# Optimization experiments

Hardware: AMD Instinct MI355X
Metric: run time of the kernel (lower is better)

## Reference

```python
import jax, jax.numpy as jnp
import numpy as np

HEADS = 16
DIM = 1024
D_K = DIM // HEADS
SEQ = 2048


def setup_inputs() -> dict:
    key = jax.random.key(0)
    ks = jax.random.split(key, 11)
    s = 1.0 / np.sqrt(DIM).astype(np.float32)
    return {
        "q": jax.random.normal(ks[0], (SEQ, DIM), jnp.float32),
        "k": jax.random.normal(ks[1], (SEQ, DIM), jnp.float32),
        "v": jax.random.normal(ks[2], (SEQ, DIM), jnp.float32),
        "Wq": jax.random.normal(ks[3], (DIM, DIM), jnp.float32) * s,
        "bq": jax.random.normal(ks[4], (DIM,), jnp.float32) * 0.01,
        "Wk": jax.random.normal(ks[5], (DIM, DIM), jnp.float32) * s,
        "bk": jax.random.normal(ks[6], (DIM,), jnp.float32) * 0.01,
        "Wv": jax.random.normal(ks[7], (DIM, DIM), jnp.float32) * s,
        "bv": jax.random.normal(ks[8], (DIM,), jnp.float32) * 0.01,
        "Wo": jax.random.normal(ks[9], (DIM, DIM), jnp.float32) * s,
        "bo": jax.random.normal(ks[10], (DIM,), jnp.float32) * 0.01,
    }


def reference(q, k, v, Wq, bq, Wk, bk, Wv, bv, Wo, bo):
    S = q.shape[0]
    # torch Linear: x @ W.T + b; view to (1, S, H, d_k) then transpose to (1, H, S, d_k)
    def proj(x, W, b):
        return (x @ W.T + b).reshape(1, S, HEADS, D_K).transpose(0, 2, 1, 3)

    qh = proj(q, Wq, bq)  # (1, H, S, d)
    kh = proj(k, Wk, bk)
    vh = proj(v, Wv, bv)

    scale = 1.0 / np.sqrt(D_K).astype(np.float32)
    scores = jnp.einsum("bhqd,bhkd->bhqk", qh, kh) * scale  # (1, H, S, S)
    # NOTE: source applies softmax over dim=1 == the HEADS axis (faithful quirk)
    attn = jax.nn.softmax(scores, axis=1)
    ctx = jnp.einsum("bhqk,bhkd->bhqd", attn, vh)  # (1, H, S, d)
    concat = ctx.transpose(0, 2, 1, 3).reshape(1, S, DIM)
    return concat @ Wo.T + bo
```

## Files before the change

kernel.cpp:

```cpp
#include <hip/hip_runtime.h>
#include <hip/hip_fp16.h>


typedef _Float16 f16;
typedef _Float16 f16x4 __attribute__((ext_vector_type(4)));
typedef _Float16 f16x8 __attribute__((ext_vector_type(8)));
typedef float    f32x4 __attribute__((ext_vector_type(4)));

#define S_LEN 2048
#define DIM   1024
#define NH    16
#define DK    64
#define SCALE 0.125f

#define MFMA(a, b, c) __builtin_amdgcn_mfma_f32_16x16x32_f16(a, b, c, 0, 0, 0)

typedef __attribute__((address_space(1))) void g_void;
typedef __attribute__((address_space(3))) void l_void;

static __device__ __forceinline__ void gload_lds16(const void* g, void* l) {
  __builtin_amdgcn_global_load_lds((g_void*)g, (l_void*)l, 16, 0, 0);
}

__global__ __launch_bounds__(256) void cvt_f32_f16(const float* __restrict__ src,
                                                   f16* __restrict__ dst, int n4) {
  int i = blockIdx.x * 256 + threadIdx.x;
  if (i < n4) {
    float4 v = ((const float4*)src)[i];
    f16x4 o = {(f16)v.x, (f16)v.y, (f16)v.z, (f16)v.w};
    ((f16x4*)dst)[i] = o;
  }
}

__global__ __launch_bounds__(256) void cvt3(const float* __restrict__ s0, const float* __restrict__ s1,
                                            const float* __restrict__ s2, f16* __restrict__ d0,
                                            f16* __restrict__ d1, f16* __restrict__ d2, int n4) {
  int z = blockIdx.y;
  const float* src = z == 0 ? s0 : z == 1 ? s1 : s2;
  f16* dst = z == 0 ? d0 : z == 1 ? d1 : d2;
  int i = blockIdx.x * 256 + threadIdx.x;
  if (i < n4) {
    float4 v = ((const float4*)src)[i];
    f16x4 o = {(f16)v.x, (f16)v.y, (f16)v.z, (f16)v.w};
    ((f16x4*)dst)[i] = o;
  }
}

__global__ __launch_bounds__(256) void cvt4(const float* __restrict__ s0, const float* __restrict__ s1,
                                            const float* __restrict__ s2, const float* __restrict__ s3,
                                            f16* __restrict__ d0, f16* __restrict__ d1,
                                            f16* __restrict__ d2, f16* __restrict__ d3, int n4) {
  int z = blockIdx.y;
  const float* src = z == 0 ? s0 : z == 1 ? s1 : z == 2 ? s2 : s3;
  f16* dst = z == 0 ? d0 : z == 1 ? d1 : z == 2 ? d2 : d3;
  int i = blockIdx.x * 256 + threadIdx.x;
  if (i < n4) {
    float4 v = ((const float4*)src)[i];
    f16x4 o = {(f16)v.x, (f16)v.y, (f16)v.z, (f16)v.w};
    ((f16x4*)dst)[i] = o;
  }
}

static __device__ __forceinline__ void gemm64_core(const f16* __restrict__ X,
                                                   const f16* __restrict__ W,
                                                   int k0, int k1, int bm, int bn,
                                                   f16* As, f16* Bs,
                                                   f32x4 (&acc)[4][2]) {
  const int tid = threadIdx.x;
  const int wv = tid >> 6;
  const int lane = tid & 63;
  const int qd = lane >> 4;
  const int l16 = lane & 15;
  const int wm = (wv & 1) * 64;
  const int wn = (wv >> 1) * 32;
  const int lr4 = lane >> 2, lc4 = lane & 3;

  const f16* gA = X + (size_t)(bm + wv * 32 + lr4) * DIM + k0 + lc4 * 8;
  const f16* gB = W + (size_t)(bn + wv * 16 + lr4) * DIM + k0 + lc4 * 8;
  f16* lA = &As[(wv * 32) * 32];
  f16* lB = &Bs[(wv * 16) * 32];

  for (int kt = k0; kt < k1; kt += 32) {
    gload_lds16(gA, lA);
    gload_lds16(gA + 16 * DIM, lA + 16 * 32);
    gload_lds16(gB, lB);
    gA += 32;
    gB += 32;
    __syncthreads();

    f16x8 af[4], bf[2];
#pragma unroll
    for (int mi = 0; mi < 4; mi++)
      af[mi] = *(const f16x8*)&As[(wm + mi * 16 + l16) * 32 + qd * 8];
#pragma unroll
    for (int ni = 0; ni < 2; ni++)
      bf[ni] = *(const f16x8*)&Bs[(wn + ni * 16 + l16) * 32 + qd * 8];
#pragma unroll
    for (int mi = 0; mi < 4; mi++)
#pragma unroll
      for (int ni = 0; ni < 2; ni++)
        acc[mi][ni] = MFMA(af[mi], bf[ni], acc[mi][ni]);
    __syncthreads();
  }
}

__global__ __launch_bounds__(256) void gemm_qkv(
    const f16* __restrict__ X0, const f16* __restrict__ X1, const f16* __restrict__ X2,
    const f16* __restrict__ W0, const f16* __restrict__ W1, const f16* __restrict__ W2,
    const float* __restrict__ b0, const float* __restrict__ b1, const float* __restrict__ b2,
    f16* __restrict__ o0, f16* __restrict__ o1, f16* __restrict__ o2) {
  __shared__ __align__(16) f16 As[128 * 32];
  __shared__ __align__(16) f16 Bs[64 * 32];
  const int z = blockIdx.z;
  const f16* X = z == 0 ? X0 : z == 1 ? X1 : X2;
  const f16* W = z == 0 ? W0 : z == 1 ? W1 : W2;
  const float* bias = z == 0 ? b0 : z == 1 ? b1 : b2;
  f16* outh = z == 0 ? o0 : z == 1 ? o1 : o2;

  const int bm = blockIdx.y * 128, bn = blockIdx.x * 64;
  f32x4 acc[4][2];
#pragma unroll
  for (int a = 0; a < 4; a++)
#pragma unroll
    for (int b = 0; b < 2; b++) acc[a][b] = (f32x4){0.f, 0.f, 0.f, 0.f};

  gemm64_core(X, W, 0, DIM, bm, bn, As, Bs, acc);

  const int tid = threadIdx.x;
  const int wv = tid >> 6, lane = tid & 63;
  const int qd = lane >> 4, l16 = lane & 15;
  const int wm = (wv & 1) * 64, wn = (wv >> 1) * 32;
#pragma unroll
  for (int mi = 0; mi < 4; mi++) {
#pragma unroll
    for (int ni = 0; ni < 2; ni++) {
      const int gm = bm + wm + mi * 16 + qd * 4;
      const int gn = bn + wn + ni * 16 + l16;
      const float bs = bias[gn];
      if (z == 2) {
        f16x4 o = {(f16)(acc[mi][ni][0] + bs), (f16)(acc[mi][ni][1] + bs),
                   (f16)(acc[mi][ni][2] + bs), (f16)(acc[mi][ni][3] + bs)};
        *(f16x4*)&outh[(size_t)gn * S_LEN + gm] = o;
      } else {
#pragma unroll
        for (int r = 0; r < 4; r++)
          outh[(size_t)(gm + r) * DIM + gn] = (f16)(acc[mi][ni][r] + bs);
      }
    }
  }
}

__global__ __launch_bounds__(256) void gemm_out(const f16* __restrict__ X,
                                                const f16* __restrict__ W,
                                                const float* __restrict__ bias,
                                                float* __restrict__ outf) {
  __shared__ __align__(16) f16 As[128 * 32];
  __shared__ __align__(16) f16 Bs[64 * 32];
  const int z = blockIdx.z;
  const int bm = blockIdx.y * 128, bn = blockIdx.x * 64;
  f32x4 acc[4][2];
#pragma unroll
  for (int a = 0; a < 4; a++)
#pragma unroll
    for (int b = 0; b < 2; b++) acc[a][b] = (f32x4){0.f, 0.f, 0.f, 0.f};

  gemm64_core(X, W, z * (DIM / 2), (z + 1) * (DIM / 2), bm, bn, As, Bs, acc);

  const int tid = threadIdx.x;
  const int wv = tid >> 6, lane = tid & 63;
  const int qd = lane >> 4, l16 = lane & 15;
  const int wm = (wv & 1) * 64, wn = (wv >> 1) * 32;
#pragma unroll
  for (int mi = 0; mi < 4; mi++) {
#pragma unroll
    for (int ni = 0; ni < 2; ni++) {
      const int gm = bm + wm + mi * 16 + qd * 4;
      const int gn = bn + wn + ni * 16 + l16;
      const float bs = z == 0 ? bias[gn] : 0.f;
#pragma unroll
      for (int r = 0; r < 4; r++)
        atomicAdd(&outf[(size_t)(gm + r) * DIM + gn], acc[mi][ni][r] + bs);
    }
  }
}

__global__ __launch_bounds__(256) void attn_denom(const f16* __restrict__ Qp,
                                                  const f16* __restrict__ Kp,
                                                  f16* __restrict__ IDn) {
  __shared__ __align__(16) f16 Qs[2][64 * 32];
  __shared__ __align__(16) f16 Ks[2][64 * 32];
  const int tid = threadIdx.x;
  const int wv = tid >> 6;
  const int lane = tid & 63;
  const int qd = lane >> 4;
  const int l16 = lane & 15;
  const int wm = (wv & 1) * 32, wn = (wv >> 1) * 32;
  const int bi = blockIdx.y * 64, bj = blockIdx.x * 64;
  const int lr4 = lane >> 2, lc4 = lane & 3;
  const int kkw = wv & 1;
  const int rw = (wv >> 1) * 32;

  f32x4 dsum[2][2];
#pragma unroll
  for (int a = 0; a < 2; a++)
#pragma unroll
    for (int b = 0; b < 2; b++) dsum[a][b] = (f32x4){0.f, 0.f, 0.f, 0.f};

  for (int h = 0; h < NH; h++) {
    const f16* gq = Qp + (size_t)(bi + rw + lr4) * DIM + h * DK + kkw * 32 + lc4 * 8;
    const f16* gk = Kp + (size_t)(bj + rw + lr4) * DIM + h * DK + kkw * 32 + lc4 * 8;
    gload_lds16(gq, &Qs[kkw][rw * 32]);
    gload_lds16(gq + 16 * DIM, &Qs[kkw][(rw + 16) * 32]);
    gload_lds16(gk, &Ks[kkw][rw * 32]);
    gload_lds16(gk + 16 * DIM, &Ks[kkw][(rw + 16) * 32]);
    __syncthreads();

    f16x8 af[2][2], bf[2][2];
#pragma unroll
    for (int mi = 0; mi < 2; mi++)
#pragma unroll
      for (int kk = 0; kk < 2; kk++)
        af[mi][kk] = *(const f16x8*)&Qs[kk][(wm + mi * 16 + l16) * 32 + qd * 8];
#pragma unroll
    for (int ni = 0; ni < 2; ni++)
#pragma unroll
      for (int kk = 0; kk < 2; kk++)
        bf[ni][kk] = *(const f16x8*)&Ks[kk][(wn + ni * 16 + l16) * 32 + qd * 8];
#pragma unroll
    for (int mi = 0; mi < 2; mi++)
#pragma unroll
      for (int ni = 0; ni < 2; ni++) {
        f32x4 s = {0.f, 0.f, 0.f, 0.f};
        s = MFMA(af[mi][0], bf[ni][0], s);
        s = MFMA(af[mi][1], bf[ni][1], s);
#pragma unroll
        for (int r = 0; r < 4; r++) dsum[mi][ni][r] += __expf(s[r] * SCALE);
      }
    __syncthreads();
  }
#pragma unroll
  for (int mi = 0; mi < 2; mi++)
#pragma unroll
    for (int ni = 0; ni < 2; ni++)
#pragma unroll
      for (int r = 0; r < 4; r++) {
        const int gi = bi + wm + mi * 16 + qd * 4 + r;
        const int gj = bj + wn + ni * 16 + l16;
        IDn[(size_t)gi * S_LEN + gj] = (f16)(1.f / dsum[mi][ni][r]);
      }
}

__global__ __launch_bounds__(256) void attn_ctx(const f16* __restrict__ Qp,
                                                const f16* __restrict__ Kp,
                                                const f16* __restrict__ Vt,
                                                const f16* __restrict__ IDn,
                                                float* __restrict__ Cp) {
  __shared__ __align__(16) f16 Ks[2][32 * 32];
  __shared__ __align__(16) f16 Vs[64 * 32];
  __shared__ __align__(16) f16 Is[128 * 32];
  __shared__ __align__(16) f16 Pl[4][32 * 32];
  const int tid = threadIdx.x;
  const int wv = tid >> 6;
  const int lane = tid & 63;
  const int qd = lane >> 4;
  const int l16 = lane & 15;
  const int h = blockIdx.y;
  const int i0 = blockIdx.x * 128;
  const int iw = i0 + wv * 32;
  const int jb = blockIdx.z * 512;
  const int lr4 = lane >> 2, lc4 = lane & 3;
  f16* pl = Pl[wv];

  f16x8 aq[2][2];
#pragma unroll
  for (int mi = 0; mi < 2; mi++)
#pragma unroll
    for (int kk = 0; kk < 2; kk++)
      aq[mi][kk] = *(const f16x8*)(Qp + (size_t)(iw + mi * 16 + l16) * DIM +
                                   h * DK + kk * 32 + qd * 8);

  f32x4 acc[2][4];
#pragma unroll
  for (int a = 0; a < 2; a++)
#pragma unroll
    for (int b = 0; b < 4; b++) acc[a][b] = (f32x4){0.f, 0.f, 0.f, 0.f};

  for (int jt = 0; jt < 16; jt++) {
    const int j0 = jb + jt * 32;
    gload_lds16(Kp + (size_t)(j0 + (wv >> 1) * 16 + lr4) * DIM + h * DK + (wv & 1) * 32 + lc4 * 8,
                &Ks[wv & 1][((wv >> 1) * 16) * 32]);
    gload_lds16(Vt + (size_t)(h * DK + wv * 16 + lr4) * S_LEN + j0 + lc4 * 8,
                &Vs[(wv * 16) * 32]);
#pragma unroll
    for (int t = 0; t < 2; t++) {
      const int row = (wv * 2 + t) * 16;
      gload_lds16(IDn + (size_t)(i0 + row + lr4) * S_LEN + j0 + lc4 * 8,
                  &Is[row * 32]);
    }
    __syncthreads();

    f16x8 bk[2][2];
#pragma unroll
    for (int ni = 0; ni < 2; ni++)
#pragma unroll
      for (int kk = 0; kk < 2; kk++)
        bk[ni][kk] = *(const f16x8*)&Ks[kk][(ni * 16 + l16) * 32 + qd * 8];
#pragma unroll
    for (int mi = 0; mi < 2; mi++)
#pragma unroll
      for (int ni = 0; ni < 2; ni++) {
        f32x4 s = {0.f, 0.f, 0.f, 0.f};
        s = MFMA(aq[mi][0], bk[ni][0], s);
        s = MFMA(aq[mi][1], bk[ni][1], s);
#pragma unroll
        for (int r = 0; r < 4; r++)
          pl[(mi * 16 + qd * 4 + r) * 32 + ni * 16 + l16] = (f16)__expf(s[r] * SCALE);
      }

    f16x8 bv[4];
#pragma unroll
    for (int nd = 0; nd < 4; nd++)
      bv[nd] = *(const f16x8*)&Vs[(nd * 16 + l16) * 32 + qd * 8];
#pragma unroll
    for (int mi = 0; mi < 2; mi++) {
      f16x8 ef = *(const f16x8*)&pl[(mi * 16 + l16) * 32 + qd * 8];
      f16x8 idn = *(const f16x8*)&Is[(wv * 32 + mi * 16 + l16) * 32 + qd * 8];
      f16x8 p = ef * idn;
#pragma unroll
      for (int nd = 0; nd < 4; nd++)
        acc[mi][nd] = MFMA(p, bv[nd], acc[mi][nd]);
    }
    __syncthreads();
  }

#pragma unroll
  for (int mi = 0; mi < 2; mi++)
#pragma unroll
    for (int nd = 0; nd < 4; nd++)
#pragma unroll
      for (int r = 0; r < 4; r++)
        atomicAdd(&Cp[(size_t)(iw + mi * 16 + qd * 4 + r) * DIM + h * DK + nd * 16 + l16],
                  acc[mi][nd][r]);
}

extern "C" void kernel_launch(void* const* d_in, const int* in_sizes, int n_in,
                              void* d_out, int out_size, void* d_ws, size_t ws_size,
                              hipStream_t stream) {
  const float* q  = (const float*)d_in[0];
  const float* k  = (const float*)d_in[1];
  const float* v  = (const float*)d_in[2];
  const float* Wq = (const float*)d_in[3];
  const float* bq = (const float*)d_in[4];
  const float* Wk = (const float*)d_in[5];
  const float* bk = (const float*)d_in[6];
  const float* Wv = (const float*)d_in[7];
  const float* bv = (const float*)d_in[8];
  const float* Wo = (const float*)d_in[9];
  const float* bo = (const float*)d_in[10];
  float* out = (float*)d_out;

  f16* w = (f16*)d_ws;
  f16* qh  = w;
  f16* kh  = qh + (size_t)S_LEN * DIM;
  f16* vh  = kh + (size_t)S_LEN * DIM;
  f16* wqh = vh + (size_t)S_LEN * DIM;
  f16* wkh = wqh + (size_t)DIM * DIM;
  f16* wvh = wkh + (size_t)DIM * DIM;
  f16* woh = wvh + (size_t)DIM * DIM;
  f16* Qp  = woh + (size_t)DIM * DIM;
  f16* Kp  = Qp + (size_t)S_LEN * DIM;
  f16* Vt  = Kp + (size_t)S_LEN * DIM;
  f16* IDn = qh;
  float* Cp = (float*)vh;
  f16* Ct  = qh;

  const int nqkv4 = S_LEN * DIM / 4, nw4 = DIM * DIM / 4;
  dim3 b256(256);
  cvt3<<<dim3(nqkv4 / 256, 3), b256, 0, stream>>>(q, k, v, qh, kh, vh, nqkv4);
  cvt4<<<dim3(nw4 / 256, 4), b256, 0, stream>>>(Wq, Wk, Wv, Wo, wqh, wkh, wvh, woh, nw4);

  gemm_qkv<<<dim3(DIM / 64, S_LEN / 128, 3), b256, 0, stream>>>(
      qh, kh, vh, wqh, wkh, wvh, bq, bk, bv, Qp, Kp, Vt);

  hipMemsetAsync(Cp, 0, (size_t)S_LEN * DIM * sizeof(float), stream);
  hipMemsetAsync(out, 0, (size_t)S_LEN * DIM * sizeof(float), stream);

  attn_denom<<<dim3(S_LEN / 64, S_LEN / 64), b256, 0, stream>>>(Qp, Kp, IDn);
  attn_ctx<<<dim3(S_LEN / 128, NH, 4), b256, 0, stream>>>(Qp, Kp, Vt, IDn, Cp);

  cvt_f32_f16<<<nqkv4 / 256, b256, 0, stream>>>(Cp, Ct, nqkv4);

  gemm_out<<<dim3(DIM / 64, S_LEN / 128, 2), b256, 0, stream>>>(Ct, woh, bo, out);
}
```

Before: 235.4 us.

## Double K-step per barrier in GEMM and attention kernels, merge conversion launches

The GEMM core, the attention-denominator kernel and the attention-context kernel now load twice as much data per synchronisation step: 64-wide K in the GEMM, two heads per iteration in attn_denom, and 64 keys per tile in attn_ctx. This halves the number of __syncthreads barriers and loop iterations, at the cost of more LDS per block. The two input conversion kernels are merged into one 10-segment launch to save a kernel launch. The larger LDS footprint may reduce occupancy.

```diff
diff --git a/kernel.cpp b/kernel.cpp
--- a/kernel.cpp
+++ b/kernel.cpp
@@ -20,6 +20,34 @@
 
 static __device__ __forceinline__ void gload_lds16(const void* g, void* l) {
   __builtin_amdgcn_global_load_lds((g_void*)g, (l_void*)l, 16, 0, 0);
+}
+
+__global__ __launch_bounds__(256) void cvt_all(
+    const float* __restrict__ q, const float* __restrict__ k, const float* __restrict__ v,
+    const float* __restrict__ Wq, const float* __restrict__ Wk, const float* __restrict__ Wv,
+    const float* __restrict__ Wo, f16* __restrict__ qh, f16* __restrict__ kh,
+    f16* __restrict__ vh, f16* __restrict__ wqh, f16* __restrict__ wkh,
+    f16* __restrict__ wvh, f16* __restrict__ woh) {
+  const size_t M = 1048576;
+  const int seg = blockIdx.y;
+  const float* src;
+  f16* dst;
+  switch (seg) {
+    case 0: src = q;      dst = qh;      break;
+    case 1: src = q + M;  dst = qh + M;  break;
+    case 2: src = k;      dst = kh;      break;
+    case 3: src = k + M;  dst = kh + M;  break;
+    case 4: src = v;      dst = vh;      break;
+    case 5: src = v + M;  dst = vh + M;  break;
+    case 6: src = Wq;     dst = wqh;     break;
+    case 7: src = Wk;     dst = wkh;     break;
+    case 8: src = Wv;     dst = wvh;     break;
+    default: src = Wo;    dst = woh;     break;
+  }
+  int i = blockIdx.x * 256 + threadIdx.x;
+  float4 vv = ((const float4*)src)[i];
+  f16x4 o = {(f16)vv.x, (f16)vv.y, (f16)vv.z, (f16)vv.w};
+  ((f16x4*)dst)[i] = o;
 }
 
 __global__ __launch_bounds__(256) void cvt_f32_f16(const float* __restrict__ src,
@@ -32,39 +60,10 @@
   }
 }
 
-__global__ __launch_bounds__(256) void cvt3(const float* __restrict__ s0, const float* __restrict__ s1,
-                                            const float* __restrict__ s2, f16* __restrict__ d0,
-                                            f16* __restrict__ d1, f16* __restrict__ d2, int n4) {
-  int z = blockIdx.y;
-  const float* src = z == 0 ? s0 : z == 1 ? s1 : s2;
-  f16* dst = z == 0 ? d0 : z == 1 ? d1 : d2;
-  int i = blockIdx.x * 256 + threadIdx.x;
-  if (i < n4) {
-    float4 v = ((const float4*)src)[i];
-    f16x4 o = {(f16)v.x, (f16)v.y, (f16)v.z, (f16)v.w};
-    ((f16x4*)dst)[i] = o;
-  }
-}
-
-__global__ __launch_bounds__(256) void cvt4(const float* __restrict__ s0, const float* __restrict__ s1,
-                                            const float* __restrict__ s2, const float* __restrict__ s3,
-                                            f16* __restrict__ d0, f16* __restrict__ d1,
-                                            f16* __restrict__ d2, f16* __restrict__ d3, int n4) {
-  int z = blockIdx.y;
-  const float* src = z == 0 ? s0 : z == 1 ? s1 : z == 2 ? s2 : s3;
-  f16* dst = z == 0 ? d0 : z == 1 ? d1 : z == 2 ? d2 : d3;
-  int i = blockIdx.x * 256 + threadIdx.x;
-  if (i < n4) {
-    float4 v = ((const float4*)src)[i];
-    f16x4 o = {(f16)v.x, (f16)v.y, (f16)v.z, (f16)v.w};
-    ((f16x4*)dst)[i] = o;
-  }
-}
-
 static __device__ __forceinline__ void gemm64_core(const f16* __restrict__ X,
                                                    const f16* __restrict__ W,
                                                    int k0, int k1, int bm, int bn,
-                                                   f16* As, f16* Bs,
+                                                   f16* As2, f16* Bs2,
                                                    f32x4 (&acc)[4][2]) {
   const int tid = threadIdx.x;
   const int wv = tid >> 6;
@@ -74,32 +73,43 @@
   const int wm = (wv & 1) * 64;
   const int wn = (wv >> 1) * 32;
   const int lr4 = lane >> 2, lc4 = lane & 3;
-
-  const f16* gA = X + (size_t)(bm + wv * 32 + lr4) * DIM + k0 + lc4 * 8;
-  const f16* gB = W + (size_t)(bn + wv * 16 + lr4) * DIM + k0 + lc4 * 8;
-  f16* lA = &As[(wv * 32) * 32];
-  f16* lB = &Bs[(wv * 16) * 32];
-
-  for (int kt = k0; kt < k1; kt += 32) {
-    gload_lds16(gA, lA);
-    gload_lds16(gA + 16 * DIM, lA + 16 * 32);
-    gload_lds16(gB, lB);
-    gA += 32;
-    gB += 32;
-    __syncthreads();
-
-    f16x8 af[4], bf[2];
+  const int kkw = wv & 1;
+  const int rgw = wv >> 1;
+
+  const f16* gA = X + (size_t)(bm + rgw * 64 + lr4) * DIM + k0 + kkw * 32 + lc4 * 8;
+  const f16* gB = W + (size_t)(bn + rgw * 32 + lr4) * DIM + k0 + kkw * 32 + lc4 * 8;
+  f16* lA = As2 + kkw * (128 * 32) + (rgw * 64) * 32;
+  f16* lB = Bs2 + kkw * (64 * 32) + (rgw * 32) * 32;
+
+  for (int kt = k0; kt < k1; kt += 64) {
+#pragma unroll
+    for (int t = 0; t < 4; t++)
+      gload_lds16(gA + t * 16 * DIM, lA + t * 16 * 32);
+#pragma unroll
+    for (int t = 0; t < 2; t++)
+      gload_lds16(gB + t * 16 * DIM, lB + t * 16 * 32);
+    gA += 64;
+    gB += 64;
+    __syncthreads();
+
+    f16x8 af[4][2], bf[2][2];
 #pragma unroll
     for (int mi = 0; mi < 4; mi++)
-      af[mi] = *(const f16x8*)&As[(wm + mi * 16 + l16) * 32 + qd * 8];
+#pragma unroll
+      for (int kk = 0; kk < 2; kk++)
+        af[mi][kk] = *(const f16x8*)&As2[kk * (128 * 32) + (wm + mi * 16 + l16) * 32 + qd * 8];
 #pragma unroll
     for (int ni = 0; ni < 2; ni++)
-      bf[ni] = *(const f16x8*)&Bs[(wn + ni * 16 + l16) * 32 + qd * 8];
+#pragma unroll
+      for (int kk = 0; kk < 2; kk++)
+        bf[ni][kk] = *(const f16x8*)&Bs2[kk * (64 * 32) + (wn + ni * 16 + l16) * 32 + qd * 8];
 #pragma unroll
     for (int mi = 0; mi < 4; mi++)
 #pragma unroll
-      for (int ni = 0; ni < 2; ni++)
-        acc[mi][ni] = MFMA(af[mi], bf[ni], acc[mi][ni]);
+      for (int ni = 0; ni < 2; ni++) {
+        acc[mi][ni] = MFMA(af[mi][0], bf[ni][0], acc[mi][ni]);
+        acc[mi][ni] = MFMA(af[mi][1], bf[ni][1], acc[mi][ni]);
+      }
     __syncthreads();
   }
 }
@@ -109,8 +119,8 @@
     const f16* __restrict__ W0, const f16* __restrict__ W1, const f16* __restrict__ W2,
     const float* __restrict__ b0, const float* __restrict__ b1, const float* __restrict__ b2,
     f16* __restrict__ o0, f16* __restrict__ o1, f16* __restrict__ o2) {
-  __shared__ __align__(16) f16 As[128 * 32];
-  __shared__ __align__(16) f16 Bs[64 * 32];
+  __shared__ __align__(16) f16 As2[2 * 128 * 32];
+  __shared__ __align__(16) f16 Bs2[2 * 64 * 32];
   const int z = blockIdx.z;
   const f16* X = z == 0 ? X0 : z == 1 ? X1 : X2;
   const f16* W = z == 0 ? W0 : z == 1 ? W1 : W2;
@@ -124,7 +134,7 @@
 #pragma unroll
     for (int b = 0; b < 2; b++) acc[a][b] = (f32x4){0.f, 0.f, 0.f, 0.f};
 
-  gemm64_core(X, W, 0, DIM, bm, bn, As, Bs, acc);
+  gemm64_core(X, W, 0, DIM, bm, bn, As2, Bs2, acc);
 
   const int tid = threadIdx.x;
   const int wv = tid >> 6, lane = tid & 63;
@@ -154,8 +164,8 @@
                                                 const f16* __restrict__ W,
                                                 const float* __restrict__ bias,
                                                 float* __restrict__ outf) {
-  __shared__ __align__(16) f16 As[128 * 32];
-  __shared__ __align__(16) f16 Bs[64 * 32];
+  __shared__ __align__(16) f16 As2[2 * 128 * 32];
+  __shared__ __align__(16) f16 Bs2[2 * 64 * 32];
   const int z = blockIdx.z;
   const int bm = blockIdx.y * 128, bn = blockIdx.x * 64;
   f32x4 acc[4][2];
@@ -164,7 +174,7 @@
 #pragma unroll
     for (int b = 0; b < 2; b++) acc[a][b] = (f32x4){0.f, 0.f, 0.f, 0.f};
 
-  gemm64_core(X, W, z * (DIM / 2), (z + 1) * (DIM / 2), bm, bn, As, Bs, acc);
+  gemm64_core(X, W, z * (DIM / 2), (z + 1) * (DIM / 2), bm, bn, As2, Bs2, acc);
 
   const int tid = threadIdx.x;
   const int wv = tid >> 6, lane = tid & 63;
@@ -187,8 +197,8 @@
 __global__ __launch_bounds__(256) void attn_denom(const f16* __restrict__ Qp,
                                                   const f16* __restrict__ Kp,
                                                   f16* __restrict__ IDn) {
-  __shared__ __align__(16) f16 Qs[2][64 * 32];
-  __shared__ __align__(16) f16 Ks[2][64 * 32];
+  __shared__ __align__(16) f16 Qs[2][2][64 * 32];
+  __shared__ __align__(16) f16 Ks[2][2][64 * 32];
   const int tid = threadIdx.x;
   const int wv = tid >> 6;
   const int lane = tid & 63;
@@ -197,8 +207,8 @@
   const int wm = (wv & 1) * 32, wn = (wv >> 1) * 32;
   const int bi = blockIdx.y * 64, bj = blockIdx.x * 64;
   const int lr4 = lane >> 2, lc4 = lane & 3;
-  const int kkw = wv & 1;
-  const int rw = (wv >> 1) * 32;
+  const int hhw = wv & 1;
+  const int kkw = wv >> 1;
 
   f32x4 dsum[2][2];
 #pragma unroll
@@ -206,36 +216,41 @@
 #pragma unroll
     for (int b = 0; b < 2; b++) dsum[a][b] = (f32x4){0.f, 0.f, 0.f, 0.f};
 
-  for (int h = 0; h < NH; h++) {
-    const f16* gq = Qp + (size_t)(bi + rw + lr4) * DIM + h * DK + kkw * 32 + lc4 * 8;
-    const f16* gk = Kp + (size_t)(bj + rw + lr4) * DIM + h * DK + kkw * 32 + lc4 * 8;
-    gload_lds16(gq, &Qs[kkw][rw * 32]);
-    gload_lds16(gq + 16 * DIM, &Qs[kkw][(rw + 16) * 32]);
-    gload_lds16(gk, &Ks[kkw][rw * 32]);
-    gload_lds16(gk + 16 * DIM, &Ks[kkw][(rw + 16) * 32]);
-    __syncthreads();
-
-    f16x8 af[2][2], bf[2][2];
-#pragma unroll
-    for (int mi = 0; mi < 2; mi++)
-#pragma unroll
-      for (int kk = 0; kk < 2; kk++)
-        af[mi][kk] = *(const f16x8*)&Qs[kk][(wm + mi * 16 + l16) * 32 + qd * 8];
-#pragma unroll
-    for (int ni = 0; ni < 2; ni++)
-#pragma unroll
-      for (int kk = 0; kk < 2; kk++)
-        bf[ni][kk] = *(const f16x8*)&Ks[kk][(wn + ni * 16 + l16) * 32 + qd * 8];
-#pragma unroll
-    for (int mi = 0; mi < 2; mi++)
-#pragma unroll
-      for (int ni = 0; ni < 2; ni++) {
-        f32x4 s = {0.f, 0.f, 0.f, 0.f};
-        s = MFMA(af[mi][0], bf[ni][0], s);
-        s = MFMA(af[mi][1], bf[ni][1], s);
-#pragma unroll
-        for (int r = 0; r < 4; r++) dsum[mi][ni][r] += __expf(s[r] * SCALE);
-      }
+  for (int h0 = 0; h0 < NH; h0 += 2) {
+    const int hcol = (h0 + hhw) * DK + kkw * 32;
+    const f16* gq = Qp + (size_t)(bi + lr4) * DIM + hcol + lc4 * 8;
+    const f16* gk = Kp + (size_t)(bj + lr4) * DIM + hcol + lc4 * 8;
+#pragma unroll
+    for (int t = 0; t < 4; t++) {
+      gload_lds16(gq + (size_t)t * 16 * DIM, &Qs[hhw][kkw][t * 16 * 32]);
+      gload_lds16(gk + (size_t)t * 16 * DIM, &Ks[hhw][kkw][t * 16 * 32]);
+    }
+    __syncthreads();
+
+#pragma unroll
+    for (int hh = 0; hh < 2; hh++) {
+      f16x8 af[2][2], bf[2][2];
+#pragma unroll
+      for (int mi = 0; mi < 2; mi++)
+#pragma unroll
+        for (int kk = 0; kk < 2; kk++)
+          af[mi][kk] = *(const f16x8*)&Qs[hh][kk][(wm + mi * 16 + l16) * 32 + qd * 8];
+#pragma unroll
+      for (int ni = 0; ni < 2; ni++)
+#pragma unroll
+        for (int kk = 0; kk < 2; kk++)
+          bf[ni][kk] = *(const f16x8*)&Ks[hh][kk][(wn + ni * 16 + l16) * 32 + qd * 8];
+#pragma unroll
+      for (int mi = 0; mi < 2; mi++)
+#pragma unroll
+        for (int ni = 0; ni < 2; ni++) {
+          f32x4 s = {0.f, 0.f, 0.f, 0.f};
+          s = MFMA(af[mi][0], bf[ni][0], s);
+          s = MFMA(af[mi][1], bf[ni][1], s);
+#pragma unroll
+          for (int r = 0; r < 4; r++) dsum[mi][ni][r] += __expf(s[r] * SCALE);
+        }
+    }
     __syncthreads();
   }
 #pragma unroll
@@ -255,9 +270,9 @@
                                                 const f16* __restrict__ Vt,
                                                 const f16* __restrict__ IDn,
                                                 float* __restrict__ Cp) {
-  __shared__ __align__(16) f16 Ks[2][32 * 32];
-  __shared__ __align__(16) f16 Vs[64 * 32];
-  __shared__ __align__(16) f16 Is[128 * 32];
+  __shared__ __align__(16) f16 Ks[2][64 * 32];
+  __shared__ __align__(16) f16 Vs[2][64 * 32];
+  __shared__ __align__(16) f16 Is[2][128 * 32];
   __shared__ __align__(16) f16 Pl[4][32 * 32];
   const int tid = threadIdx.x;
   const int wv = tid >> 6;
@@ -269,6 +284,8 @@
   const int iw = i0 + wv * 32;
   const int jb = blockIdx.z * 512;
   const int lr4 = lane >> 2, lc4 = lane & 3;
+  const int sw = wv & 1;
+  const int gw = wv >> 1;
   f16* pl = Pl[wv];
 
   f16x8 aq[2][2];
@@ -285,50 +302,55 @@
 #pragma unroll
     for (int b = 0; b < 4; b++) acc[a][b] = (f32x4){0.f, 0.f, 0.f, 0.f};
 
-  for (int jt = 0; jt < 16; jt++) {
-    const int j0 = jb + jt * 32;
-    gload_lds16(Kp + (size_t)(j0 + (wv >> 1) * 16 + lr4) * DIM + h * DK + (wv & 1) * 32 + lc4 * 8,
-                &Ks[wv & 1][((wv >> 1) * 16) * 32]);
-    gload_lds16(Vt + (size_t)(h * DK + wv * 16 + lr4) * S_LEN + j0 + lc4 * 8,
-                &Vs[(wv * 16) * 32]);
-#pragma unroll
-    for (int t = 0; t < 2; t++) {
-      const int row = (wv * 2 + t) * 16;
-      gload_lds16(IDn + (size_t)(i0 + row + lr4) * S_LEN + j0 + lc4 * 8,
-                  &Is[row * 32]);
-    }
-    __syncthreads();
-
-    f16x8 bk[2][2];
-#pragma unroll
-    for (int ni = 0; ni < 2; ni++)
-#pragma unroll
-      for (int kk = 0; kk < 2; kk++)
-        bk[ni][kk] = *(const f16x8*)&Ks[kk][(ni * 16 + l16) * 32 + qd * 8];
-#pragma unroll
-    for (int mi = 0; mi < 2; mi++)
-#pragma unroll
-      for (int ni = 0; ni < 2; ni++) {
-        f32x4 s = {0.f, 0.f, 0.f, 0.f};
-        s = MFMA(aq[mi][0], bk[ni][0], s);
-        s = MFMA(aq[mi][1], bk[ni][1], s);
-#pragma unroll
-        for (int r = 0; r < 4; r++)
-          pl[(mi * 16 + qd * 4 + r) * 32 + ni * 16 + l16] = (f16)__expf(s[r] * SCALE);
+  for (int jt = 0; jt < 8; jt++) {
+    const int j0 = jb + jt * 64;
+#pragma unroll
+    for (int t = 0; t < 2; t++)
+      gload_lds16(Kp + (size_t)(j0 + gw * 32 + t * 16 + lr4) * DIM + h * DK + sw * 32 + lc4 * 8,
+                  &Ks[sw][(gw * 32 + t * 16) * 32]);
+#pragma unroll
+    for (int t = 0; t < 2; t++)
+      gload_lds16(Vt + (size_t)(h * DK + gw * 32 + t * 16 + lr4) * S_LEN + j0 + sw * 32 + lc4 * 8,
+                  &Vs[sw][(gw * 32 + t * 16) * 32]);
+#pragma unroll
+    for (int t = 0; t < 4; t++)
+      gload_lds16(IDn + (size_t)(i0 + gw * 64 + t * 16 + lr4) * S_LEN + j0 + sw * 32 + lc4 * 8,
+                  &Is[sw][(gw * 64 + t * 16) * 32]);
+    __syncthreads();
+
+#pragma unroll
+    for (int sub = 0; sub < 2; sub++) {
+      f16x8 bk[2][2];
+#pragma unroll
+      for (int ni = 0; ni < 2; ni++)
+#pragma unroll
+        for (int kk = 0; kk < 2; kk++)
+          bk[ni][kk] = *(const f16x8*)&Ks[kk][(sub * 32 + ni * 16 + l16) * 32 + qd * 8];
+#pragma unroll
+      for (int mi = 0; mi < 2; mi++)
+#pragma unroll
+        for (int ni = 0; ni < 2; ni++) {
+          f32x4 s = {0.f, 0.f, 0.f, 0.f};
+          s = MFMA(aq[mi][0], bk[ni][0], s);
+          s = MFMA(aq[mi][1], bk[ni][1], s);
+#pragma unroll
+          for (int r = 0; r < 4; r++)
+            pl[(mi * 16 + qd * 4 + r) * 32 + ni * 16 + l16] = (f16)__expf(s[r] * SCALE);
+        }
+
+      f16x8 bv[4];
+#pragma unroll
+      for (int nd = 0; nd < 4; nd++)
+        bv[nd] = *(const f16x8*)&Vs[sub][(nd * 16 + l16) * 32 + qd * 8];
+#pragma unroll
+      for (int mi = 0; mi < 2; mi++) {
+        f16x8 ef = *(const f16x8*)&pl[(mi * 16 + l16) * 32 + qd * 8];
+        f16x8 idn = *(const f16x8*)&Is[sub][(wv * 32 + mi * 16 + l16) * 32 + qd * 8];
+        f16x8 p = ef * idn;
+#pragma unroll
+        for (int nd = 0; nd < 4; nd++)
+          acc[mi][nd] = MFMA(p, bv[nd], acc[mi][nd]);
       }
-
-    f16x8 bv[4];
-#pragma unroll
-    for (int nd = 0; nd < 4; nd++)
-      bv[nd] = *(const f16x8*)&Vs[(nd * 16 + l16) * 32 + qd * 8];
-#pragma unroll
-    for (int mi = 0; mi < 2; mi++) {
-      f16x8 ef = *(const f16x8*)&pl[(mi * 16 + l16) * 32 + qd * 8];
-      f16x8 idn = *(const f16x8*)&Is[(wv * 32 + mi * 16 + l16) * 32 + qd * 8];
-      f16x8 p = ef * idn;
-#pragma unroll
-      for (int nd = 0; nd < 4; nd++)
-        acc[mi][nd] = MFMA(p, bv[nd], acc[mi][nd]);
     }
     __syncthreads();
   }
@@ -374,10 +396,9 @@
   float* Cp = (float*)vh;
   f16* Ct  = qh;
 
-  const int nqkv4 = S_LEN * DIM / 4, nw4 = DIM * DIM / 4;
   dim3 b256(256);
-  cvt3<<<dim3(nqkv4 / 256, 3), b256, 0, stream>>>(q, k, v, qh, kh, vh, nqkv4);
-  cvt4<<<dim3(nw4 / 256, 4), b256, 0, stream>>>(Wq, Wk, Wv, Wo, wqh, wkh, wvh, woh, nw4);
+  cvt_all<<<dim3(1024, 10), b256, 0, stream>>>(q, k, v, Wq, Wk, Wv, Wo,
+                                               qh, kh, vh, wqh, wkh, wvh, woh);
 
   gemm_qkv<<<dim3(DIM / 64, S_LEN / 128, 3), b256, 0, stream>>>(
       qh, kh, vh, wqh, wkh, wvh, bq, bk, bv, Qp, Kp, Vt);
@@ -388,6 +409,7 @@
   attn_denom<<<dim3(S_LEN / 64, S_LEN / 64), b256, 0, stream>>>(Qp, Kp, IDn);
   attn_ctx<<<dim3(S_LEN / 128, NH, 4), b256, 0, stream>>>(Qp, Kp, Vt, IDn, Cp);
 
+  const int nqkv4 = S_LEN * DIM / 4;
   cvt_f32_f16<<<nqkv4 / 256, b256, 0, stream>>>(Cp, Ct, nqkv4);
 
   gemm_out<<<dim3(DIM / 64, S_LEN / 128, 2), b256, 0, stream>>>(Ct, woh, bo, out);
```

After: 233.3 us. Within noise of the previous version (-0.9%).
